# Kernel optimization log

Hardware: AMD Instinct MI355X
Metric: run time of the kernel (lower is better)

## Reference

```python
import jax, jax.numpy as jnp
import numpy as np

D_MODEL = 1024
NHEADS = 16
E_HEAD = D_MODEL // NHEADS  # 64
ROPE_BASE = 10000.0


def _rope_cos_sin(L, dim, base, dtype):
    # dim = E_head (even); inv_freq over pairs, GPT-NeoX half-split convention
    inv_freq = 1.0 / (base ** (jnp.arange(0, dim, 2, dtype=jnp.float32) / dim))
    pos = jnp.arange(L, dtype=jnp.float32)
    freqs = pos[:, None] * inv_freq[None, :]  # [L, dim/2]
    return jnp.cos(freqs).astype(dtype), jnp.sin(freqs).astype(dtype)


def _apply_rope(t, cos, sin):
    # t: [B, H, L, Dh]; rotate-half formulation
    d2 = t.shape[-1] // 2
    t1, t2 = t[..., :d2], t[..., d2:]
    return jnp.concatenate([t1 * cos - t2 * sin, t1 * sin + t2 * cos], axis=-1)


def setup_inputs() -> dict:
    key = jax.random.key(0)
    ks = jax.random.split(key, 5)
    B, L = 4, 2048
    x = jax.random.normal(ks[0], (B, L, D_MODEL), dtype=jnp.float32)
    s_in = 1.0 / np.sqrt(D_MODEL)
    W_packed = jax.random.normal(ks[1], (3 * D_MODEL, D_MODEL), dtype=jnp.float32) * s_in
    b_packed = jax.random.normal(ks[2], (3 * D_MODEL,), dtype=jnp.float32) * 0.02
    W_out = jax.random.normal(ks[3], (D_MODEL, D_MODEL), dtype=jnp.float32) * s_in
    b_out = jax.random.normal(ks[4], (D_MODEL,), dtype=jnp.float32) * 0.02
    return {"x": x, "W_packed": W_packed, "b_packed": b_packed, "W_out": W_out, "b_out": b_out}


def reference(x, W_packed, b_packed, W_out, b_out):
    B, L, _ = x.shape
    # 1) packed QKV projection (query is key is value path)
    qkv = jnp.einsum('ble,fe->blf', x, W_packed) + b_packed  # [B, L, 3*D]
    q, k, v = jnp.split(qkv, 3, axis=-1)
    # 2) split heads -> [B, H, L, Dh]
    def heads(t):
        return t.reshape(B, L, NHEADS, E_HEAD).transpose(0, 2, 1, 3)
    q, k, v = heads(q), heads(k), heads(v)
    # 3) RoPE on q, k
    cos, sin = _rope_cos_sin(L, E_HEAD, ROPE_BASE, x.dtype)
    q = _apply_rope(q, cos, sin)
    k = _apply_rope(k, cos, sin)
    # 4) SDPA (non-causal, no dropout)
    scale = 1.0 / np.sqrt(E_HEAD)
    scores = jnp.einsum('bhqd,bhkd->bhqk', q, k) * scale
    attn = jax.nn.softmax(scores, axis=-1)
    out = jnp.einsum('bhqk,bhkd->bhqd', attn, v)
    # 5) merge heads + output projection
    out = out.transpose(0, 2, 1, 3).reshape(B, L, D_MODEL)
    return jnp.einsum('bld,ed->ble', out, W_out) + b_out
```

## Files before the change

### kernel.cpp

```cpp
#include <hip/hip_runtime.h>
#include <hip/hip_bf16.h>
#include <stdint.h>

#define L_SEQ 2048
#define NB    4
#define NH    16
#define EH    64
#define DM    1024
#define MTOT  (NB * L_SEQ)

typedef __attribute__((ext_vector_type(8))) short bf16x8;
typedef __attribute__((ext_vector_type(4))) float f32x4;
typedef __attribute__((ext_vector_type(16))) float f32x16;
typedef __attribute__((ext_vector_type(2))) unsigned uint2v;

static __device__ __forceinline__ float bf2f(short u) {
    union { unsigned int i; float f; } c;
    c.i = ((unsigned int)(unsigned short)u) << 16;
    return c.f;
}
static __device__ __forceinline__ short f2bf(float f) {
    union { float f; unsigned int i; } c; c.f = f;
    unsigned int x = c.i;
    unsigned int r = (x + 0x7fffu + ((x >> 16) & 1u)) >> 16;
    return (short)(unsigned short)r;
}
static __device__ __forceinline__ unsigned cvtpk(float lo, float hi) {
    unsigned r;
    asm volatile("v_cvt_pk_bf16_f32 %0, %1, %2" : "=v"(r) : "v"(lo), "v"(hi));
    return r;
}
static __device__ __forceinline__ float pairmax(float x) {
    union { float f; unsigned u; } c; c.f = x;
    uint2v r = __builtin_amdgcn_permlane32_swap(c.u, c.u, false, false);
    union { unsigned u; float f; } a, b; a.u = r[0]; b.u = r[1];
    return fmaxf(a.f, b.f);
}

static __device__ __forceinline__ void gload_lds16(const void* g, void* lds) {
    __builtin_amdgcn_global_load_lds(
        (const __attribute__((address_space(1))) unsigned int*)g,
        (__attribute__((address_space(3))) unsigned int*)lds, 16, 0, 0);
}

__global__ __launch_bounds__(256) void cvt3_k(const float* __restrict__ x,
                                              const float* __restrict__ wp,
                                              const float* __restrict__ wo,
                                              short* __restrict__ xb,
                                              short* __restrict__ wpb,
                                              short* __restrict__ wob) {
    int bid = blockIdx.x;
    const float* src; short* dst; int i;
    if (bid < 8192)       { src = x;  dst = xb;  i = bid * 256 + threadIdx.x; }
    else if (bid < 11264) { src = wp; dst = wpb; i = (bid - 8192) * 256 + threadIdx.x; }
    else                  { src = wo; dst = wob; i = (bid - 11264) * 256 + threadIdx.x; }
    float4 v = ((const float4*)src)[i];
    short4 o;
    o.x = f2bf(v.x); o.y = f2bf(v.y); o.z = f2bf(v.z); o.w = f2bf(v.w);
    ((short4*)dst)[i] = o;
}

__global__ __launch_bounds__(256) void rope_table_k(float* __restrict__ tab) {
    int i = blockIdx.x * 256 + threadIdx.x;
    int l = i >> 5, d = i & 31;
    float inv = powf(10000.0f, -(float)d * (1.0f / 32.0f));
    float fr = (float)l * inv;
    tab[i]         = cosf(fr);
    tab[65536 + i] = sinf(fr);
}

template<int OUTBF16, int NBX>
__global__ __launch_bounds__(512, 2) void gemm256_k(const short* __restrict__ A,
                                                    const short* __restrict__ Bt,
                                                    const float* __restrict__ bias,
                                                    void* __restrict__ Cv) {
    __shared__ short lds[2][2][256 * 32];
    const int t = threadIdx.x;
    const int w = t >> 6, l = t & 63;
    const int wm = w >> 2, wn = w & 3;
    const int lr = l & 15, lh = l >> 4;
    const int N = NBX * 256;

    const int nblk = NBX * 32;
    int fid = blockIdx.x + blockIdx.y * NBX;
    int swz = (fid & 7) * (nblk >> 3) + (fid >> 3);
    const int n0 = (swz % NBX) * 256;
    const int m0 = (swz / NBX) * 256;

    const int lrow = l >> 2;
    const int schunk = (l & 3) ^ ((l >> 3) & 3);

    const short* Ag = A + (size_t)(m0 + lrow) * 1024 + schunk * 8;
    const short* Bg = Bt + (size_t)(n0 + lrow) * 1024 + schunk * 8;

    auto STAGE = [&](int kt, int buf) {
#pragma unroll
        for (int j = 0; j < 2; ++j) {
            const int r = (w * 2 + j) * 16;
            gload_lds16(Ag + (size_t)r * 1024 + kt * 32, &lds[buf][0][r * 32]);
            gload_lds16(Bg + (size_t)r * 1024 + kt * 32, &lds[buf][1][r * 32]);
        }
    };

    f32x4 acc[8][4] = {};

    STAGE(0, 0);
    STAGE(1, 1);
    asm volatile("s_waitcnt vmcnt(4)" ::: "memory");
    __builtin_amdgcn_s_barrier();

    const int fch = (lh ^ ((lr >> 1) & 3)) << 3;

#pragma unroll 2
    for (int kt = 0; kt < 32; ++kt) {
        const int c = kt & 1;
        const short* Al = &lds[c][0][0];
        const short* Bl = &lds[c][1][0];

        bf16x8 bfr[4], af[8];
#pragma unroll
        for (int nj = 0; nj < 4; ++nj)
            bfr[nj] = *(const bf16x8*)(Bl + (wn * 64 + nj * 16 + lr) * 32 + fch);
#pragma unroll
        for (int mi = 0; mi < 8; ++mi)
            af[mi] = *(const bf16x8*)(Al + (wm * 128 + mi * 16 + lr) * 32 + fch);

        __builtin_amdgcn_s_setprio(1);
#pragma unroll
        for (int mi = 0; mi < 8; ++mi)
#pragma unroll
            for (int nj = 0; nj < 4; ++nj)
                acc[mi][nj] = __builtin_amdgcn_mfma_f32_16x16x32_bf16(
                    af[mi], bfr[nj], acc[mi][nj], 0, 0, 0);
        __builtin_amdgcn_s_setprio(0);

        asm volatile("s_waitcnt lgkmcnt(0)" ::: "memory");
        __builtin_amdgcn_s_barrier();
        if (kt + 2 < 32) {
            STAGE(kt + 2, c);
            asm volatile("s_waitcnt vmcnt(4)" ::: "memory");
        } else {
            asm volatile("s_waitcnt vmcnt(0)" ::: "memory");
        }
        __builtin_amdgcn_s_barrier();
    }

#pragma unroll
    for (int mi = 0; mi < 8; ++mi) {
#pragma unroll
        for (int nj = 0; nj < 4; ++nj) {
            const int row = m0 + wm * 128 + mi * 16 + lh * 4;
            const int col = n0 + wn * 64 + nj * 16 + lr;
            const float bsv = bias[col];
#pragma unroll
            for (int j = 0; j < 4; ++j) {
                float v = acc[mi][nj][j] + bsv;
                if (OUTBF16)
                    ((short*)Cv)[(size_t)(row + j) * N + col] = f2bf(v);
                else
                    ((float*)Cv)[(size_t)(row + j) * N + col] = v;
            }
        }
    }
}

__global__ __launch_bounds__(256) void rope_scatter_k(const short* __restrict__ qkv,
                                                      const float* __restrict__ tab,
                                                      short* __restrict__ Q,
                                                      short* __restrict__ Kd) {
    int idx = blockIdx.x * 256 + threadIdx.x;
    int d = idx & 31;
    int h = (idx >> 5) & 15;
    int bl = idx >> 9;
    int l = bl & (L_SEQ - 1);
    int b = bl >> 11;
    float c = tab[l * 32 + d], s = tab[65536 + l * 32 + d];
    const short* row = qkv + (size_t)bl * 3072;
    float q1 = bf2f(row[h * 64 + d]);
    float q2 = bf2f(row[h * 64 + d + 32]);
    float k1 = bf2f(row[1024 + h * 64 + d]);
    float k2 = bf2f(row[1024 + h * 64 + d + 32]);
    size_t ob = ((size_t)((b * 16 + h) * 2048 + l)) * 64;
    const float sc = 0.18033688011112042f;
    Q[ob + d]       = f2bf((q1 * c - q2 * s) * sc);
    Q[ob + d + 32]  = f2bf((q1 * s + q2 * c) * sc);
    int r7 = l & 7;
    int c1 = ((d >> 3) ^ r7) * 8 + (d & 7);
    int c2 = (((d >> 3) | 4) ^ r7) * 8 + (d & 7);
    Kd[ob + c1] = f2bf(k1 * c - k2 * s);
    Kd[ob + c2] = f2bf(k1 * s + k2 * c);
}

__global__ __launch_bounds__(256) void v_trans_k(const short* __restrict__ qkv,
                                                 short* __restrict__ Vt) {
    __shared__ short tile[64 * 65];
    int bh = blockIdx.y;
    int l0 = blockIdx.x * 64;
    int t = threadIdx.x;
    int b = bh >> 4, h = bh & 15;
#pragma unroll
    for (int i = 0; i < 16; i++) {
        int l = i * 4 + (t >> 6);
        int d = t & 63;
        tile[d * 65 + l] = qkv[(size_t)(b * 2048 + l0 + l) * 3072 + 2048 + h * 64 + d];
    }
    __syncthreads();
#pragma unroll
    for (int i = 0; i < 16; i++) {
        int d = i * 4 + (t >> 6);
        int lx = t & 63;
        int cl = (lx & ~0xC) | ((lx & 4) << 1) | ((lx & 8) >> 1);
        int lp = l0 | ((((cl >> 3) ^ (d & 7)) << 3)) | (cl & 7);
        Vt[(size_t)(bh * 64 + d) * 2048 + lp] = tile[d * 65 + lx];
    }
}

__global__ __launch_bounds__(512, 4) void attn_k(const short* __restrict__ Qg,
                                                 const short* __restrict__ Kg,
                                                 const short* __restrict__ Vt,
                                                 short* __restrict__ O) {
    __shared__ short Ks[2][64 * 64];
    __shared__ short Vs[2][64 * 64];
    const int t = threadIdx.x;
    const int w = t >> 6, l = t & 63;
    const int q = l & 31, hi = l >> 5;
    const int r7 = l & 7;

    const int od = blockIdx.x + blockIdx.y * 8;
    const int qblk = (od >> 3) & 7;
    const int bh = (od & 7) * 8 + (od >> 6);
    const int q0 = qblk * 256;

    const short* Qb = Qg + (size_t)bh * (2048 * 64);
    const short* Kb = Kg + (size_t)bh * (2048 * 64);
    const short* Vb = Vt + (size_t)bh * (64 * 2048);

    const int qrow = q0 + w * 32 + q;
    bf16x8 qf[4];
#pragma unroll
    for (int ds = 0; ds < 4; ds++)
        qf[ds] = *(const bf16x8*)(Qb + (size_t)qrow * 64 + ds * 16 + hi * 8);

    const short one_bf = (short)0x3F80;
    const bf16x8 ones = {one_bf, one_bf, one_bf, one_bf, one_bf, one_bf, one_bf, one_bf};

    f32x16 o0 = {}, o1 = {}, os = {};
    float m = -1e30f;

    const int grow = w * 8 + (l >> 3);
    const int gcol = r7 * 8;

    gload_lds16(Kb + (size_t)grow * 64 + gcol, &Ks[0][w * 512]);
    gload_lds16(Vb + (size_t)grow * 2048 + gcol, &Vs[0][w * 512]);
    __syncthreads();

    for (int it = 0; it < 32; ++it) {
        const int cur = it & 1;
        const short* Kc = &Ks[cur][0];
        const short* Vc = &Vs[cur][0];
        if (it < 31) {
            const int kn = (it + 1) * 64;
            gload_lds16(Kb + (size_t)(kn + grow) * 64 + gcol, &Ks[cur ^ 1][w * 512]);
            gload_lds16(Vb + (size_t)grow * 2048 + kn + gcol, &Vs[cur ^ 1][w * 512]);
        }

        f32x16 s0 = {}, s1 = {};
#pragma unroll
        for (int ds = 0; ds < 4; ds++) {
            const int ch = ((ds << 1) | hi) ^ r7;
            bf16x8 k0f = *(const bf16x8*)(Kc + q * 64 + ch * 8);
            bf16x8 k1f = *(const bf16x8*)(Kc + (32 + q) * 64 + ch * 8);
            __builtin_amdgcn_s_setprio(1);
            s0 = __builtin_amdgcn_mfma_f32_32x32x16_bf16(k0f, qf[ds], s0, 0, 0, 0);
            s1 = __builtin_amdgcn_mfma_f32_32x32x16_bf16(k1f, qf[ds], s1, 0, 0, 0);
            __builtin_amdgcn_s_setprio(0);
        }

        float a[8];
#pragma unroll
        for (int i = 0; i < 8; i++)
            a[i] = fmaxf(fmaxf(s0[i], s0[i + 8]), fmaxf(s1[i], s1[i + 8]));
        float pm = pairmax(fmaxf(
            fmaxf(fmaxf(a[0], a[1]), fmaxf(a[2], a[3])),
            fmaxf(fmaxf(a[4], a[5]), fmaxf(a[6], a[7]))));

        if (__any((int)(pm > m + 8.0f))) {
            float mn = fmaxf(m, pm);
            float sc = __builtin_amdgcn_exp2f(m - mn);
#pragma unroll
            for (int r = 0; r < 16; r++) { o0[r] *= sc; o1[r] *= sc; os[r] *= sc; }
            m = mn;
        }

#pragma unroll
        for (int r = 0; r < 16; r++) {
            s0[r] = __builtin_amdgcn_exp2f(s0[r] - m);
            s1[r] = __builtin_amdgcn_exp2f(s1[r] - m);
        }

        bf16x8 pf[4];
        {
            union { unsigned u[4]; bf16x8 v; } f;
            f.u[0] = cvtpk(s0[0], s0[1]);  f.u[1] = cvtpk(s0[2], s0[3]);
            f.u[2] = cvtpk(s0[4], s0[5]);  f.u[3] = cvtpk(s0[6], s0[7]);
            pf[0] = f.v;
            f.u[0] = cvtpk(s0[8], s0[9]);  f.u[1] = cvtpk(s0[10], s0[11]);
            f.u[2] = cvtpk(s0[12], s0[13]); f.u[3] = cvtpk(s0[14], s0[15]);
            pf[1] = f.v;
            f.u[0] = cvtpk(s1[0], s1[1]);  f.u[1] = cvtpk(s1[2], s1[3]);
            f.u[2] = cvtpk(s1[4], s1[5]);  f.u[3] = cvtpk(s1[6], s1[7]);
            pf[2] = f.v;
            f.u[0] = cvtpk(s1[8], s1[9]);  f.u[1] = cvtpk(s1[10], s1[11]);
            f.u[2] = cvtpk(s1[12], s1[13]); f.u[3] = cvtpk(s1[14], s1[15]);
            pf[3] = f.v;
        }

#pragma unroll
        for (int ks = 0; ks < 4; ks++) {
            const int ch = ((ks << 1) | hi) ^ r7;
            bf16x8 v0f = *(const bf16x8*)(Vc + q * 64 + ch * 8);
            bf16x8 v1f = *(const bf16x8*)(Vc + (32 + q) * 64 + ch * 8);
            __builtin_amdgcn_s_setprio(1);
            o0 = __builtin_amdgcn_mfma_f32_32x32x16_bf16(v0f, pf[ks], o0, 0, 0, 0);
            o1 = __builtin_amdgcn_mfma_f32_32x32x16_bf16(v1f, pf[ks], o1, 0, 0, 0);
            os = __builtin_amdgcn_mfma_f32_32x32x16_bf16(ones, pf[ks], os, 0, 0, 0);
            __builtin_amdgcn_s_setprio(0);
        }

        __syncthreads();
    }

    const float inv = 1.0f / os[0];
    const int b = bh >> 4, h = bh & 15;
    short* Orow = O + (size_t)(b * 2048 + qrow) * 1024 + h * 64;
#pragma unroll
    for (int g = 0; g < 4; g++) {
        unsigned w0 = cvtpk(o0[g * 4 + 0] * inv, o0[g * 4 + 1] * inv);
        unsigned w1 = cvtpk(o0[g * 4 + 2] * inv, o0[g * 4 + 3] * inv);
        unsigned long long p0 = (unsigned long long)w0 | ((unsigned long long)w1 << 32);
        *(unsigned long long*)(Orow + g * 8 + hi * 4) = p0;
        unsigned w2 = cvtpk(o1[g * 4 + 0] * inv, o1[g * 4 + 1] * inv);
        unsigned w3 = cvtpk(o1[g * 4 + 2] * inv, o1[g * 4 + 3] * inv);
        unsigned long long p1 = (unsigned long long)w2 | ((unsigned long long)w3 << 32);
        *(unsigned long long*)(Orow + 32 + g * 8 + hi * 4) = p1;
    }
}

extern "C" void kernel_launch(void* const* d_in, const int* in_sizes, int n_in,
                              void* d_out, int out_size, void* d_ws, size_t ws_size,
                              hipStream_t stream) {
    const float* x  = (const float*)d_in[0];
    const float* Wp = (const float*)d_in[1];
    const float* bp = (const float*)d_in[2];
    const float* Wo = (const float*)d_in[3];
    const float* bo = (const float*)d_in[4];

    char* ws = (char*)d_ws;
    const size_t SZ_XB  = (size_t)MTOT * DM * 2;
    const size_t SZ_WPB = (size_t)3 * DM * DM * 2;
    const size_t SZ_WOB = (size_t)DM * DM * 2;
    const size_t SZ_QKV = (size_t)MTOT * 3 * DM * 2;
    const size_t SZ_BHLE = (size_t)MTOT * DM * 2;

    short* xb   = (short*)(ws);
    short* wpb  = (short*)(ws + SZ_XB);
    short* wob  = (short*)(ws + SZ_XB + SZ_WPB);
    short* qkvb = (short*)(ws + SZ_XB + SZ_WPB + SZ_WOB);
    short* Qb   = (short*)(ws + SZ_XB + SZ_WPB + SZ_WOB + SZ_QKV);
    short* Kb   = (short*)(ws + SZ_XB + SZ_WPB + SZ_WOB + SZ_QKV + SZ_BHLE);
    short* Vtb  = (short*)(ws + SZ_XB + SZ_WPB + SZ_WOB + SZ_QKV + 2 * SZ_BHLE);
    short* Ob   = (short*)(ws + SZ_XB + SZ_WPB + SZ_WOB + SZ_QKV + 3 * SZ_BHLE);
    float* tab  = (float*)(ws + SZ_XB + SZ_WPB + SZ_WOB + SZ_QKV + 4 * SZ_BHLE);

    cvt3_k<<<12288, 256, 0, stream>>>(x, Wp, Wo, xb, wpb, wob);
    rope_table_k<<<256, 256, 0, stream>>>(tab);

    gemm256_k<1, 12><<<dim3(12, 32), 512, 0, stream>>>(xb, wpb, bp, qkvb);

    rope_scatter_k<<<16384, 256, 0, stream>>>(qkvb, tab, Qb, Kb);
    v_trans_k<<<dim3(32, 64), 256, 0, stream>>>(qkvb, Vtb);

    attn_k<<<dim3(8, 64), 512, 0, stream>>>(Qb, Kb, Vtb, Ob);

    gemm256_k<0, 4><<<dim3(4, 32), 512, 0, stream>>>(Ob, wob, bo, d_out);
}
```

Baseline: 220.7 us.

## Triple-buffer attention K/V loads and use smaller-tile output projection GEMM

The attention kernel moves from double to triple buffering of K/V tiles in LDS. It prefetches two tiles ahead and replaces the full __syncthreads with explicit vmcnt waits plus a barrier, so global loads overlap more compute. Launch bounds drop to 2 blocks per CU to fit the larger LDS footprint. The output projection swaps the 256-tile GEMM (128 blocks) for a new 128x128-tile kernel with 512 blocks, improving CU fill on the small N=1024 GEMM at the cost of more operand traffic per FLOP.

Result: no change. 216.9 us (-1.7%).

```diff
diff --git a/kernel.cpp b/kernel.cpp
--- a/kernel.cpp
+++ b/kernel.cpp
@@ -160,6 +160,67 @@
                 else
                     ((float*)Cv)[(size_t)(row + j) * N + col] = v;
             }
+        }
+    }
+}
+
+__global__ __launch_bounds__(256) void gemm_out_k(const short* __restrict__ A,
+                                                  const short* __restrict__ Bt,
+                                                  const float* __restrict__ bias,
+                                                  float* __restrict__ Cv,
+                                                  int N, int K) {
+    __shared__ short As[128 * 64];
+    __shared__ short Bs[128 * 64];
+    const int t = threadIdx.x;
+    const int w = t >> 6, l = t & 63;
+    const int wr = w >> 1, wc = w & 1;
+    const int lr = l & 15, lh = l >> 4;
+    const int m0 = blockIdx.y * 128, n0 = blockIdx.x * 128;
+    const int srow = t >> 3;
+    const int scol = (t & 7) * 8;
+
+    f32x4 acc[4][4] = {};
+
+    const short* Ab = A + (size_t)(m0 + srow) * K + scol;
+    const short* Bb = Bt + (size_t)(n0 + srow) * K + scol;
+
+    for (int k0 = 0; k0 < K; k0 += 64) {
+        __syncthreads();
+#pragma unroll
+        for (int i = 0; i < 4; i++) {
+            gload_lds16(Ab + (size_t)(i * 32) * K + k0, As + i * 2048 + w * 512);
+            gload_lds16(Bb + (size_t)(i * 32) * K + k0, Bs + i * 2048 + w * 512);
+        }
+        __syncthreads();
+#pragma unroll
+        for (int kk = 0; kk < 2; kk++) {
+            bf16x8 af[4], bfr[4];
+#pragma unroll
+            for (int mi = 0; mi < 4; mi++)
+                af[mi] = *(const bf16x8*)(As + (wr * 64 + mi * 16 + lr) * 64 + kk * 32 + lh * 8);
+#pragma unroll
+            for (int nj = 0; nj < 4; nj++)
+                bfr[nj] = *(const bf16x8*)(Bs + (wc * 64 + nj * 16 + lr) * 64 + kk * 32 + lh * 8);
+            __builtin_amdgcn_s_setprio(1);
+#pragma unroll
+            for (int mi = 0; mi < 4; mi++)
+#pragma unroll
+                for (int nj = 0; nj < 4; nj++)
+                    acc[mi][nj] = __builtin_amdgcn_mfma_f32_16x16x32_bf16(
+                        af[mi], bfr[nj], acc[mi][nj], 0, 0, 0);
+            __builtin_amdgcn_s_setprio(0);
+        }
+    }
+#pragma unroll
+    for (int mi = 0; mi < 4; mi++) {
+#pragma unroll
+        for (int nj = 0; nj < 4; nj++) {
+            const int row = m0 + wr * 64 + mi * 16 + lh * 4;
+            const int col = n0 + wc * 64 + nj * 16 + lr;
+            const float bsv = bias[col];
+#pragma unroll
+            for (int j = 0; j < 4; j++)
+                Cv[(size_t)(row + j) * N + col] = acc[mi][nj][j] + bsv;
         }
     }
 }
@@ -215,12 +276,12 @@
     }
 }
 
-__global__ __launch_bounds__(512, 4) void attn_k(const short* __restrict__ Qg,
+__global__ __launch_bounds__(512, 2) void attn_k(const short* __restrict__ Qg,
                                                  const short* __restrict__ Kg,
                                                  const short* __restrict__ Vt,
                                                  short* __restrict__ O) {
-    __shared__ short Ks[2][64 * 64];
-    __shared__ short Vs[2][64 * 64];
+    __shared__ short Ks[3][64 * 64];
+    __shared__ short Vs[3][64 * 64];
     const int t = threadIdx.x;
     const int w = t >> 6, l = t & 63;
     const int q = l & 31, hi = l >> 5;
@@ -250,18 +311,22 @@
     const int grow = w * 8 + (l >> 3);
     const int gcol = r7 * 8;
 
-    gload_lds16(Kb + (size_t)grow * 64 + gcol, &Ks[0][w * 512]);
-    gload_lds16(Vb + (size_t)grow * 2048 + gcol, &Vs[0][w * 512]);
-    __syncthreads();
+    gload_lds16(Kb + (size_t)grow * 64 + gcol,        &Ks[0][w * 512]);
+    gload_lds16(Vb + (size_t)grow * 2048 + gcol,      &Vs[0][w * 512]);
+    gload_lds16(Kb + (size_t)(64 + grow) * 64 + gcol, &Ks[1][w * 512]);
+    gload_lds16(Vb + (size_t)grow * 2048 + 64 + gcol, &Vs[1][w * 512]);
+    asm volatile("s_waitcnt vmcnt(2)" ::: "memory");
+    __builtin_amdgcn_s_barrier();
+
+    const short* Kc = &Ks[0][0];  const short* Vc = &Vs[0][0];
+    const short* Kn = &Ks[1][0];  const short* Vn = &Vs[1][0];
+    short*       Kf = &Ks[2][0];  short*       Vf = &Vs[2][0];
 
     for (int it = 0; it < 32; ++it) {
-        const int cur = it & 1;
-        const short* Kc = &Ks[cur][0];
-        const short* Vc = &Vs[cur][0];
-        if (it < 31) {
-            const int kn = (it + 1) * 64;
-            gload_lds16(Kb + (size_t)(kn + grow) * 64 + gcol, &Ks[cur ^ 1][w * 512]);
-            gload_lds16(Vb + (size_t)grow * 2048 + kn + gcol, &Vs[cur ^ 1][w * 512]);
+        if (it < 30) {
+            const int kn = (it + 2) * 64;
+            gload_lds16(Kb + (size_t)(kn + grow) * 64 + gcol, Kf + w * 512);
+            gload_lds16(Vb + (size_t)grow * 2048 + kn + gcol, Vf + w * 512);
         }
 
         f32x16 s0 = {}, s1 = {};
@@ -327,7 +392,13 @@
             __builtin_amdgcn_s_setprio(0);
         }
 
-        __syncthreads();
+        asm volatile("s_waitcnt lgkmcnt(0)" ::: "memory");
+        if (it < 30) asm volatile("s_waitcnt vmcnt(2)" ::: "memory");
+        else         asm volatile("s_waitcnt vmcnt(0)" ::: "memory");
+        __builtin_amdgcn_s_barrier();
+
+        const short* tk = Kc; Kc = Kn; Kn = Kf; Kf = (short*)tk;
+        const short* tv = Vc; Vc = Vn; Vn = Vf; Vf = (short*)tv;
     }
 
     const float inv = 1.0f / os[0];
@@ -382,5 +453,5 @@
 
     attn_k<<<dim3(8, 64), 512, 0, stream>>>(Qb, Kb, Vtb, Ob);
 
-    gemm256_k<0, 4><<<dim3(4, 32), 512, 0, stream>>>(Ob, wob, bo, d_out);
-}
+    gemm_out_k<<<dim3(8, 64), 256, 0, stream>>>(Ob, wob, bo, (float*)d_out, DM, DM);
+}
```
